# Performance work log

Hardware: AMD Instinct MI355X
Metric: run time of the kernel (lower is better)

## Reference

```python
import jax, jax.numpy as jnp
import numpy as np

QMAX = 255.0  # uint8 range used by KVQuantizer


def setup_inputs() -> dict:
    key = jax.random.key(0)
    k1, k2 = jax.random.split(key)
    B, KVH, D, S = 1, 8, 128, 8192
    keys = jax.random.normal(k1, (B, KVH, 1, D, S), dtype=jnp.float32)
    values = jax.random.normal(k2, (B, KVH, 1, S, D), dtype=jnp.float32)
    return {"keys": keys, "values": values, "mask": 1, "ids_len": S, "kv_seq_len": S}


def _quantize_block(x, axis):
    # torch.aminmax(x, dim=axis, keepdim=True)
    block_min = jnp.min(x, axis=axis, keepdims=True)
    block_max = jnp.max(x, axis=axis, keepdims=True)
    scale = (block_max - block_min) * (1.0 / QMAX)
    x_packed = jnp.round((x - block_min) / scale)  # F16 path: stays float
    # USE_FLOAT16_SCALE_BIAS=True -> half precision scale/bias
    return x_packed, scale.astype(jnp.float16), block_min.astype(jnp.float16)


def reference(keys, values, mask, ids_len, kv_seq_len):
    # causal mask: (1 - tril(ones)) * -128, sliced [:ids_len, :kv_seq_len], * mask, .float()
    row = jnp.arange(ids_len)[:, None]
    col = jnp.arange(kv_seq_len)[None, :]
    attn = (jnp.where(col > row, jnp.int32(-128), jnp.int32(0)) * jnp.int32(mask)).astype(jnp.float32)
    attn = attn[None, None, None]  # [1,1,1,ids_len,kv_seq_len]

    # per-layer KV-cache quantization (keys blocked over head_dim axis -2, values over -1)
    k_packed, k_scale, k_bias = _quantize_block(keys, -2)
    v_packed, v_scale, v_bias = _quantize_block(values, -1)
    return (attn, k_packed, k_scale, k_bias, v_packed, jnp.swapaxes(v_scale, -1, -2), v_bias)
```

## Files before the change

### kernel.cpp

```cpp
#include <hip/hip_runtime.h>
#include <hip/hip_fp16.h>

#define HH 8
#define DD 128
#define SS 8192

__global__ __launch_bounds__(256) void attn_kernel(const int* __restrict__ maskp,
                                                   float* __restrict__ out) {
    const float hi = (float)(-128 * (*maskp));
    int idx = blockIdx.x * 256 + threadIdx.x;
    int r  = idx >> 11;
    int c  = (idx & 2047) << 2;
    float4 v;
    v.x = (c + 0 > r) ? hi : 0.0f;
    v.y = (c + 1 > r) ? hi : 0.0f;
    v.z = (c + 2 > r) ? hi : 0.0f;
    v.w = (c + 3 > r) ? hi : 0.0f;
    ((float4*)out)[idx] = v;
}

__global__ __launch_bounds__(256) void keys_kernel(const float* __restrict__ keys,
                                                   float* __restrict__ kp,
                                                   float* __restrict__ ks,
                                                   float* __restrict__ kb) {
    const int h  = blockIdx.x >> 7;
    const int s0 = (blockIdx.x & 127) << 6;
    const int sl = threadIdx.x & 63;
    const int td = threadIdx.x >> 6;

    const float* base = keys + (size_t)h * DD * SS + s0 + sl;
    float val[32];
    float mn = 3.0e38f, mx = -3.0e38f;
#pragma unroll
    for (int j = 0; j < 32; ++j) {
        float v = base[(size_t)(td * 32 + j) * SS];
        val[j] = v;
        mn = fminf(mn, v);
        mx = fmaxf(mx, v);
    }

    __shared__ float smin[4][64], smax[4][64], sscale[64], sbias[64];
    smin[td][sl] = mn;
    smax[td][sl] = mx;
    __syncthreads();
    if (td == 0) {
        float m0 = fminf(fminf(smin[0][sl], smin[1][sl]), fminf(smin[2][sl], smin[3][sl]));
        float M0 = fmaxf(fmaxf(smax[0][sl], smax[1][sl]), fmaxf(smax[2][sl], smax[3][sl]));
        float scale = (M0 - m0) * (1.0f / 255.0f);
        sscale[sl] = scale;
        sbias[sl]  = m0;
        int o = h * SS + s0 + sl;
        ks[o] = __half2float(__float2half(scale));
        kb[o] = __half2float(__float2half(m0));
    }
    __syncthreads();
    const float scale = sscale[sl];
    const float bias  = sbias[sl];
    float* ob = kp + (size_t)h * DD * SS + s0 + sl;
#pragma unroll
    for (int j = 0; j < 32; ++j) {
        ob[(size_t)(td * 32 + j) * SS] = rintf((val[j] - bias) / scale);
    }
}

__global__ __launch_bounds__(256) void vals_kernel(const float* __restrict__ vals,
                                                   float* __restrict__ vp,
                                                   float* __restrict__ vs,
                                                   float* __restrict__ vb) {
    const int d4 = threadIdx.x & 31;
    const int rr = threadIdx.x >> 5;
    const int R  = blockIdx.x * 8 + rr;

    const float4 v = ((const float4*)vals)[R * 32 + d4];
    float mn = fminf(fminf(v.x, v.y), fminf(v.z, v.w));
    float mx = fmaxf(fmaxf(v.x, v.y), fmaxf(v.z, v.w));
#pragma unroll
    for (int off = 16; off >= 1; off >>= 1) {
        mn = fminf(mn, __shfl_xor(mn, off));
        mx = fmaxf(mx, __shfl_xor(mx, off));
    }
    const float scale = (mx - mn) * (1.0f / 255.0f);
    if (d4 == 0) {
        vs[R] = __half2float(__float2half(scale));
        vb[R] = __half2float(__float2half(mn));
    }
    float4 o;
    o.x = rintf((v.x - mn) / scale);
    o.y = rintf((v.y - mn) / scale);
    o.z = rintf((v.z - mn) / scale);
    o.w = rintf((v.w - mn) / scale);
    ((float4*)vp)[R * 32 + d4] = o;
}

extern "C" void kernel_launch(void* const* d_in, const int* in_sizes, int n_in,
                              void* d_out, int out_size, void* d_ws, size_t ws_size,
                              hipStream_t stream) {
    const float* keys  = (const float*)d_in[0];
    const float* vals  = (const float*)d_in[1];
    const int*   maskp = (const int*)d_in[2];

    float* out  = (float*)d_out;
    float* attn = out;
    float* kp   = attn + 67108864;
    float* ks   = kp   + 8388608;
    float* kb   = ks   + 65536;
    float* vp   = kb   + 65536;
    float* vs   = vp   + 8388608;
    float* vb   = vs   + 65536;

    attn_kernel<<<dim3(SS * (SS / 4) / 256), dim3(256), 0, stream>>>(maskp, attn);
    keys_kernel<<<dim3(HH * (SS / 64)), dim3(256), 0, stream>>>(keys, kp, ks, kb);
    vals_kernel<<<dim3(HH * SS / 8), dim3(256), 0, stream>>>(vals, vp, vs, vb);
}
```

Baseline: 375.3 us.

## Fuse mask, key and value quantization into one interleaved kernel with vector nontemporal IO

The three launches are merged into a single kernel. Block indices are interleaved so that each group of 25 blocks holds one key block, eight value blocks and sixteen mask-writing blocks, which mixes read-heavy and write-only work across the device. The key path now loads and stores four adjacent sequence positions per thread as float4 instead of scalar strided accesses, and it reduces min and max through a larger shared-memory tree. All global loads and stores use nontemporal builtins so that streaming data bypasses the cache. The cost is branch divergence at block granularity and a heavier key reduction.

Result: slower. 383.5 us (+2.2%).

```diff
diff --git a/kernel.cpp b/kernel.cpp
--- a/kernel.cpp
+++ b/kernel.cpp
@@ -5,91 +5,118 @@
 #define DD 128
 #define SS 8192
 
-__global__ __launch_bounds__(256) void attn_kernel(const int* __restrict__ maskp,
-                                                   float* __restrict__ out) {
-    const float hi = (float)(-128 * (*maskp));
-    int idx = blockIdx.x * 256 + threadIdx.x;
-    int r  = idx >> 11;
-    int c  = (idx & 2047) << 2;
-    float4 v;
-    v.x = (c + 0 > r) ? hi : 0.0f;
-    v.y = (c + 1 > r) ? hi : 0.0f;
-    v.z = (c + 2 > r) ? hi : 0.0f;
-    v.w = (c + 3 > r) ? hi : 0.0f;
-    ((float4*)out)[idx] = v;
-}
+typedef float f32x4 __attribute__((ext_vector_type(4)));
 
-__global__ __launch_bounds__(256) void keys_kernel(const float* __restrict__ keys,
-                                                   float* __restrict__ kp,
-                                                   float* __restrict__ ks,
-                                                   float* __restrict__ kb) {
-    const int h  = blockIdx.x >> 7;
-    const int s0 = (blockIdx.x & 127) << 6;
-    const int sl = threadIdx.x & 63;
-    const int td = threadIdx.x >> 6;
+#define GROUPS 1024
+#define BLOCKS (GROUPS * 25)
 
-    const float* base = keys + (size_t)h * DD * SS + s0 + sl;
-    float val[32];
-    float mn = 3.0e38f, mx = -3.0e38f;
+__global__ __launch_bounds__(256) void fused_kernel(
+    const float* __restrict__ keys, const float* __restrict__ vals,
+    const int* __restrict__ maskp,
+    float* __restrict__ attn, float* __restrict__ kp, float* __restrict__ ks,
+    float* __restrict__ kb, float* __restrict__ vp, float* __restrict__ vs,
+    float* __restrict__ vb)
+{
+    const int tid = threadIdx.x;
+    const int b   = blockIdx.x;
+    const int g   = b / 25;
+    const int rem = b - g * 25;
+
+    if (rem == 0) {
+        const int h  = g >> 7;
+        const int s0 = (g & 127) << 6;
+        const int sq = tid & 15;
+        const int dg = tid >> 4;
+
+        const float* base = keys + (size_t)h * DD * SS + (size_t)dg * 8 * SS + s0 + sq * 4;
+        f32x4 v[8];
+        f32x4 mn4, mx4;
+        mn4.x = mn4.y = mn4.z = mn4.w = 3.0e38f;
+        mx4.x = mx4.y = mx4.z = mx4.w = -3.0e38f;
 #pragma unroll
-    for (int j = 0; j < 32; ++j) {
-        float v = base[(size_t)(td * 32 + j) * SS];
-        val[j] = v;
-        mn = fminf(mn, v);
-        mx = fmaxf(mx, v);
+        for (int j = 0; j < 8; ++j) {
+            v[j] = __builtin_nontemporal_load((const f32x4*)(base + (size_t)j * SS));
+            mn4.x = fminf(mn4.x, v[j].x); mx4.x = fmaxf(mx4.x, v[j].x);
+            mn4.y = fminf(mn4.y, v[j].y); mx4.y = fmaxf(mx4.y, v[j].y);
+            mn4.z = fminf(mn4.z, v[j].z); mx4.z = fmaxf(mx4.z, v[j].z);
+            mn4.w = fminf(mn4.w, v[j].w); mx4.w = fmaxf(mx4.w, v[j].w);
+        }
+
+        __shared__ f32x4 smn[16][16], smx[16][16];
+        __shared__ float ssc[64], sbi[64];
+        smn[dg][sq] = mn4;
+        smx[dg][sq] = mx4;
+        __syncthreads();
+        if (tid < 64) {
+            const int q = tid >> 2, cmp = tid & 3;
+            float m = 3.0e38f, M = -3.0e38f;
+#pragma unroll
+            for (int gg = 0; gg < 16; ++gg) {
+                m = fminf(m, ((const float*)&smn[gg][q])[cmp]);
+                M = fmaxf(M, ((const float*)&smx[gg][q])[cmp]);
+            }
+            const float scale = (M - m) * (1.0f / 255.0f);
+            ssc[tid] = scale;
+            sbi[tid] = m;
+            const int o = h * SS + s0 + tid;
+            ks[o] = __half2float(__float2half(scale));
+            kb[o] = __half2float(__float2half(m));
+        }
+        __syncthreads();
+        const f32x4 sc = *(const f32x4*)&ssc[sq * 4];
+        const f32x4 bi = *(const f32x4*)&sbi[sq * 4];
+        float* ob = kp + (size_t)h * DD * SS + (size_t)dg * 8 * SS + s0 + sq * 4;
+#pragma unroll
+        for (int j = 0; j < 8; ++j) {
+            f32x4 o;
+            o.x = rintf((v[j].x - bi.x) / sc.x);
+            o.y = rintf((v[j].y - bi.y) / sc.y);
+            o.z = rintf((v[j].z - bi.z) / sc.z);
+            o.w = rintf((v[j].w - bi.w) / sc.w);
+            __builtin_nontemporal_store(o, (f32x4*)(ob + (size_t)j * SS));
+        }
+    } else if (rem <= 8) {
+        const int vbi = g * 8 + (rem - 1);
+        const int d4 = tid & 31;
+        const int rr = tid >> 5;
+        const int R  = vbi * 8 + rr;
+
+        const f32x4 v = __builtin_nontemporal_load((const f32x4*)vals + (size_t)R * 32 + d4);
+        float mn = fminf(fminf(v.x, v.y), fminf(v.z, v.w));
+        float mx = fmaxf(fmaxf(v.x, v.y), fmaxf(v.z, v.w));
+#pragma unroll
+        for (int off = 16; off >= 1; off >>= 1) {
+            mn = fminf(mn, __shfl_xor(mn, off));
+            mx = fmaxf(mx, __shfl_xor(mx, off));
+        }
+        const float scale = (mx - mn) * (1.0f / 255.0f);
+        if (d4 == 0) {
+            vs[R] = __half2float(__float2half(scale));
+            vb[R] = __half2float(__float2half(mn));
+        }
+        f32x4 o;
+        o.x = rintf((v.x - mn) / scale);
+        o.y = rintf((v.y - mn) / scale);
+        o.z = rintf((v.z - mn) / scale);
+        o.w = rintf((v.w - mn) / scale);
+        __builtin_nontemporal_store(o, (f32x4*)vp + (size_t)R * 32 + d4);
+    } else {
+        const int a = g * 16 + (rem - 9);
+        const float hi = (float)(-128 * (*maskp));
+        const int base = a * 1024 + tid;
+#pragma unroll
+        for (int ch = 0; ch < 4; ++ch) {
+            const int idx = base + ch * 256;
+            const int r = idx >> 11;
+            const int c = (idx & 2047) << 2;
+            f32x4 v;
+            v.x = (c + 0 > r) ? hi : 0.0f;
+            v.y = (c + 1 > r) ? hi : 0.0f;
+            v.z = (c + 2 > r) ? hi : 0.0f;
+            v.w = (c + 3 > r) ? hi : 0.0f;
+            __builtin_nontemporal_store(v, (f32x4*)attn + idx);
+        }
     }
-
-    __shared__ float smin[4][64], smax[4][64], sscale[64], sbias[64];
-    smin[td][sl] = mn;
-    smax[td][sl] = mx;
-    __syncthreads();
-    if (td == 0) {
-        float m0 = fminf(fminf(smin[0][sl], smin[1][sl]), fminf(smin[2][sl], smin[3][sl]));
-        float M0 = fmaxf(fmaxf(smax[0][sl], smax[1][sl]), fmaxf(smax[2][sl], smax[3][sl]));
-        float scale = (M0 - m0) * (1.0f / 255.0f);
-        sscale[sl] = scale;
-        sbias[sl]  = m0;
-        int o = h * SS + s0 + sl;
-        ks[o] = __half2float(__float2half(scale));
-        kb[o] = __half2float(__float2half(m0));
-    }
-    __syncthreads();
-    const float scale = sscale[sl];
-    const float bias  = sbias[sl];
-    float* ob = kp + (size_t)h * DD * SS + s0 + sl;
-#pragma unroll
-    for (int j = 0; j < 32; ++j) {
-        ob[(size_t)(td * 32 + j) * SS] = rintf((val[j] - bias) / scale);
-    }
-}
-
-__global__ __launch_bounds__(256) void vals_kernel(const float* __restrict__ vals,
-                                                   float* __restrict__ vp,
-                                                   float* __restrict__ vs,
-                                                   float* __restrict__ vb) {
-    const int d4 = threadIdx.x & 31;
-    const int rr = threadIdx.x >> 5;
-    const int R  = blockIdx.x * 8 + rr;
-
-    const float4 v = ((const float4*)vals)[R * 32 + d4];
-    float mn = fminf(fminf(v.x, v.y), fminf(v.z, v.w));
-    float mx = fmaxf(fmaxf(v.x, v.y), fmaxf(v.z, v.w));
-#pragma unroll
-    for (int off = 16; off >= 1; off >>= 1) {
-        mn = fminf(mn, __shfl_xor(mn, off));
-        mx = fmaxf(mx, __shfl_xor(mx, off));
-    }
-    const float scale = (mx - mn) * (1.0f / 255.0f);
-    if (d4 == 0) {
-        vs[R] = __half2float(__float2half(scale));
-        vb[R] = __half2float(__float2half(mn));
-    }
-    float4 o;
-    o.x = rintf((v.x - mn) / scale);
-    o.y = rintf((v.y - mn) / scale);
-    o.z = rintf((v.z - mn) / scale);
-    o.w = rintf((v.w - mn) / scale);
-    ((float4*)vp)[R * 32 + d4] = o;
 }
 
 extern "C" void kernel_launch(void* const* d_in, const int* in_sizes, int n_in,
@@ -108,7 +135,6 @@
     float* vs   = vp   + 8388608;
     float* vb   = vs   + 65536;
 
-    attn_kernel<<<dim3(SS * (SS / 4) / 256), dim3(256), 0, stream>>>(maskp, attn);
-    keys_kernel<<<dim3(HH * (SS / 64)), dim3(256), 0, stream>>>(keys, kp, ks, kb);
-    vals_kernel<<<dim3(HH * SS / 8), dim3(256), 0, stream>>>(vals, vp, vs, vb);
+    fused_kernel<<<dim3(BLOCKS), dim3(256), 0, stream>>>(keys, vals, maskp,
+                                                         attn, kp, ks, kb, vp, vs, vb);
 }
```
